# Kernel optimization log

Measured on AMD Instinct MI355X. Metric: run time of the kernel, lower is better.

The kernel has to match this reference:

```python
import jax, jax.numpy as jnp
import numpy as np

N = 512      # nodes
E = 512      # edges = nb-graph nodes
M = 16384    # nb-graph edges
FIN = 64     # in_node_nf
HID = 128    # hidden_nf
D = 32       # VTV_coord_nf (positional-encoding width)


def _silu(v):
    return v * jax.nn.sigmoid(v)


def _mlp(v, w1, b1, w2, b2):
    # 2-layer MLP with SiLU (matches MLP(in, out, [hidden]))
    return _silu(v @ w1 + b1) @ w2 + b2


def setup_inputs() -> dict:
    key = jax.random.key(0)
    ks = jax.random.split(key, 32)

    def lin(k, i, o, scale=None):
        s = (1.0 / np.sqrt(i)) if scale is None else scale
        return jax.random.normal(k, (i, o), dtype=jnp.float32) * jnp.float32(s)

    inp = {}
    inp['h'] = jax.random.normal(ks[0], (N, FIN), dtype=jnp.float32)
    inp['x'] = jax.random.normal(ks[1], (N, 3), dtype=jnp.float32)
    inp['edges'] = jax.random.randint(ks[2], (2, E), 0, N)
    inp['nb_edge'] = jax.random.randint(ks[3], (2, M), 0, E)
    inp['edge_attr'] = jax.random.normal(ks[4], (E, 4), dtype=jnp.float32)
    inp['nb_num_nodes'] = E  # python int (static)
    # edge_encoder: MLP(2*FIN -> HID -> FIN)
    inp['ew1'] = lin(ks[5], 2 * FIN, HID); inp['eb1'] = jnp.zeros((HID,), jnp.float32)
    inp['ew2'] = lin(ks[6], HID, FIN);     inp['eb2'] = jnp.zeros((FIN,), jnp.float32)
    # PPGN mlp1 / mlp2: MLP(D+FIN -> HID -> FIN)
    inp['p1w1'] = lin(ks[7], D + FIN, HID); inp['p1b1'] = jnp.zeros((HID,), jnp.float32)
    inp['p1w2'] = lin(ks[8], HID, FIN);     inp['p1b2'] = jnp.zeros((FIN,), jnp.float32)
    inp['p2w1'] = lin(ks[9], D + FIN, HID); inp['p2b1'] = jnp.zeros((HID,), jnp.float32)
    inp['p2w2'] = lin(ks[10], HID, FIN);    inp['p2b2'] = jnp.zeros((FIN,), jnp.float32)
    # PPGN output mlp: MLP(D+FIN+FIN -> HID -> FIN) on concat(skip, matmul)
    inp['p3w1'] = lin(ks[11], D + 2 * FIN, HID); inp['p3b1'] = jnp.zeros((HID,), jnp.float32)
    inp['p3w2'] = lin(ks[12], HID, FIN);         inp['p3b2'] = jnp.zeros((FIN,), jnp.float32)
    # IGN 2->1: linear over 5 basis ops
    inp['ign_w'] = lin(ks[13], 5 * FIN, FIN); inp['ign_b'] = jnp.zeros((FIN,), jnp.float32)
    # coord_mlp: Linear(FIN,HID), SiLU, Linear(HID,1,bias=False) with tiny init
    inp['cw1'] = lin(ks[14], FIN, HID); inp['cb1'] = jnp.zeros((HID,), jnp.float32)
    inp['cw2'] = lin(ks[15], HID, 1, scale=0.001)
    # node_dec: MLP(FIN -> HID -> FIN)
    inp['ndw1'] = lin(ks[16], FIN, HID); inp['ndb1'] = jnp.zeros((HID,), jnp.float32)
    inp['ndw2'] = lin(ks[17], HID, FIN); inp['ndb2'] = jnp.zeros((FIN,), jnp.float32)
    return inp


def reference(h, x, edges, nb_edge, edge_attr, nb_num_nodes,
              ew1, eb1, ew2, eb2,
              p1w1, p1b1, p1w2, p1b2,
              p2w1, p2b1, p2w2, p2b2,
              p3w1, p3b1, p3w2, p3b2,
              ign_w, ign_b,
              cw1, cb1, cw2,
              ndw1, ndb1, ndw2, ndb2):
    rows, cols = edges[0], edges[1]
    coord_diff = x[rows] - x[cols]                      # [E,3]
    nbr, nbc = nb_edge[0], nb_edge[1]
    # VTV: inner product of the two relative-position vectors of paired edges
    vtv = jnp.sum(coord_diff[nbr] * coord_diff[nbc], axis=-1)   # [M]
    # sinusoidal positional encoding, a_scale = D/2
    half = D // 2
    div_term = jnp.exp(jnp.log(jnp.float32(10000.0)) * (2.0 * jnp.arange(half, dtype=jnp.float32) / D))
    ang = vtv[:, None] * jnp.float32(D / 2) / div_term          # [M, D/2]
    pe = jnp.stack([jnp.sin(ang), jnp.cos(ang)], axis=-1).reshape(vtv.shape[0], D)
    # node-pair features per original edge
    efn = _mlp(jnp.concatenate([h[rows], h[cols]], axis=1), ew1, eb1, ew2, eb2)  # [E,FIN]
    nb_feat = jnp.concatenate([pe, efn[nbr] * efn[nbc]], axis=1)                 # [M, D+FIN]
    # densify nb-graph 2-tensor and run PPGN block
    En = nb_num_nodes
    T = jnp.zeros((En, En, nb_feat.shape[1]), dtype=nb_feat.dtype).at[nbr, nbc].add(nb_feat)
    m1 = _mlp(T, p1w1, p1b1, p1w2, p1b2)                 # [En,En,FIN]
    m2 = _mlp(T, p2w1, p2b1, p2w2, p2b2)
    mult = jnp.einsum('ikf,kjf->ijf', m1, m2)            # feature-wise matmul
    Tout = _mlp(jnp.concatenate([T, mult], axis=-1), p3w1, p3b1, p3w2, p3b2)
    # IGN 2->1: diag, row-sum, col-sum, total-sum, trace (broadcast)
    idx = jnp.arange(En)
    diag = Tout[idx, idx]                                # [En,FIN]
    rowsum = Tout.sum(axis=1)
    colsum = Tout.sum(axis=0)
    tot = jnp.broadcast_to(Tout.sum(axis=(0, 1)), diag.shape)
    tr = jnp.broadcast_to(diag.sum(axis=0), diag.shape)
    nb_t1 = jnp.concatenate([diag, rowsum, colsum, tot, tr], axis=1) @ ign_w + ign_b  # [En,FIN]
    # coord update: weighted coord_diff, segment-mean over source node
    w = _silu(nb_t1 @ cw1 + cb1) @ cw2                   # [E,1]
    trans = coord_diff * w
    Nn = x.shape[0]
    seg = jax.ops.segment_sum(trans, rows, num_segments=Nn)
    cnt = jax.ops.segment_sum(jnp.ones((rows.shape[0], 1), trans.dtype), rows, num_segments=Nn)
    x_new = x + seg / jnp.clip(cnt, 1.0)
    # node update: scatter_add edge features then residual MLP
    nb_t0 = jax.ops.segment_sum(nb_t1, rows, num_segments=Nn)
    h_new = h + _mlp(nb_t0, ndw1, ndb1, ndw2, ndb2)
    return (h_new, x_new, edge_attr)
```

## Files before the change

kernel.cpp:

```cpp
#include <hip/hip_runtime.h>
#include <hip/hip_bf16.h>

#define NN   512
#define EE   512
#define MM   16384

typedef float v4f __attribute__((ext_vector_type(4)));
typedef short short8v __attribute__((ext_vector_type(8)));

__device__ __forceinline__ float silu_f(float v) { return v / (1.0f + __expf(-v)); }

__global__ __launch_bounds__(128) void k_edge(
    const float* __restrict__ h, const float* __restrict__ x,
    const int* __restrict__ edges,
    const float* __restrict__ ew1, const float* __restrict__ eb1,
    const float* __restrict__ ew2, const float* __restrict__ eb2,
    float* __restrict__ coord_diff, float* __restrict__ efn) {
  __shared__ float hin[128];
  __shared__ float hs[128];
  int e = blockIdx.x;
  int t = threadIdx.x;
  int r = edges[e], c = edges[EE + e];
  if (t < 3) coord_diff[e * 3 + t] = x[r * 3 + t] - x[c * 3 + t];
  if (t < 64) { hin[t] = h[r * 64 + t]; hin[64 + t] = h[c * 64 + t]; }
  __syncthreads();
  float acc = eb1[t];
  for (int k = 0; k < 128; ++k) acc += hin[k] * ew1[k * 128 + t];
  hs[t] = silu_f(acc);
  __syncthreads();
  if (t < 64) {
    float o = eb2[t];
    for (int k = 0; k < 128; ++k) o += hs[k] * ew2[k * 64 + t];
    efn[e * 64 + t] = o;
  }
}

__global__ __launch_bounds__(128) void k_consts(
    const float* __restrict__ p1b1, const float* __restrict__ p1w2, const float* __restrict__ p1b2,
    const float* __restrict__ p2b1, const float* __restrict__ p2w2, const float* __restrict__ p2b2,
    float* __restrict__ c1, float* __restrict__ c2) {
  __shared__ float h1[128], h2[128];
  int t = threadIdx.x;
  h1[t] = silu_f(p1b1[t]); h2[t] = silu_f(p2b1[t]);
  __syncthreads();
  if (t < 64) {
    float a1 = p1b2[t], a2 = p2b2[t];
    for (int k = 0; k < 128; ++k) { a1 += h1[k] * p1w2[k * 64 + t]; a2 += h2[k] * p2w2[k * 64 + t]; }
    c1[t] = a1; c2[t] = a2;
  }
}

__global__ __launch_bounds__(256) void k_prep(const float* __restrict__ p3w1,
                                              __hip_bfloat16* __restrict__ Wt) {
  int e = blockIdx.x * 256 + threadIdx.x;
  int hh = e >> 6, f = e & 63;
  Wt[hh * 64 + f] = __float2bfloat16(p3w1[(96 + f) * 128 + hh]);
}

__global__ __launch_bounds__(256) void k_mark(const int* __restrict__ nb_edge,
                                              int* __restrict__ slotmap) {
  int m = blockIdx.x * 256 + threadIdx.x;
  if (m >= MM) return;
  int cell = nb_edge[m] * 512 + nb_edge[MM + m];
  atomicCAS(&slotmap[cell], -1, -2);
}

__global__ __launch_bounds__(256) void k_compact(int* __restrict__ slotmap,
                                                 int* __restrict__ cells,
                                                 int* __restrict__ nC) {
  int cell = blockIdx.x * 256 + threadIdx.x;
  if (slotmap[cell] != -2) return;
  int s = atomicAdd(nC, 1);
  slotmap[cell] = s;
  cells[s] = cell;
}

__global__ __launch_bounds__(192) void k_scatterT(
    const int* __restrict__ nb_edge, const int* __restrict__ slotmap,
    const float* __restrict__ coord_diff, const float* __restrict__ efn,
    float* __restrict__ Tc) {
  int t = threadIdx.x;
  int sub = (t >= 96) ? 1 : 0;
  int c = t - sub * 96;
  int m = blockIdx.x * 2 + sub;
  int a = nb_edge[m], b = nb_edge[MM + m];
  int s = slotmap[a * 512 + b];
  float val;
  if (c < 32) {
    float vtv = coord_diff[a * 3 + 0] * coord_diff[b * 3 + 0]
              + coord_diff[a * 3 + 1] * coord_diff[b * 3 + 1]
              + coord_diff[a * 3 + 2] * coord_diff[b * 3 + 2];
    int i = c >> 1;
    float ang = vtv * 16.0f * __expf(-0.57564627324851143f * (float)i);
    val = (c & 1) ? cosf(ang) : sinf(ang);
  } else {
    int f = c - 32;
    val = efn[a * 64 + f] * efn[b * 64 + f];
  }
  atomicAdd(&Tc[s * 96 + c], val);
}

__global__ __launch_bounds__(128) void k_mlp96b(
    const int* __restrict__ cells, const int* __restrict__ nC, const float* __restrict__ Tc,
    const float* __restrict__ w11, const float* __restrict__ b11,
    const float* __restrict__ w12, const float* __restrict__ b12,
    const float* __restrict__ w21, const float* __restrict__ b21,
    const float* __restrict__ w22, const float* __restrict__ b22,
    const float* __restrict__ c1, const float* __restrict__ c2,
    const float* __restrict__ p3w1,
    __hip_bfloat16* __restrict__ D1d, __hip_bfloat16* __restrict__ D2dT,
    float* __restrict__ A, float* __restrict__ B,
    float* __restrict__ TWc) {
  __shared__ float xsT[96 * 8];
  __shared__ float hid[8][128];
  __shared__ int cl[8];
  int t = threadIdx.x;
  int nc = *nC;
  int s0 = blockIdx.x * 8;
  if (s0 >= nc) return;
  for (int e = t; e < 768; e += 128) xsT[(e % 96) * 8 + e / 96] = Tc[s0 * 96 + e];
  if (t < 8) cl[t] = (s0 + t < nc) ? cells[s0 + t] : 0;
  __syncthreads();
  float tw[8], a1[8], a2[8];
#pragma unroll
  for (int c = 0; c < 8; ++c) { tw[c] = 0.f; a1[c] = b11[t]; a2[c] = b21[t]; }
  for (int k = 0; k < 96; ++k) {
    float wt = p3w1[k * 128 + t];
    float w1v = w11[k * 128 + t];
    float w2v = w21[k * 128 + t];
    float4 xlo = *(const float4*)&xsT[k * 8];
    float4 xhi = *(const float4*)&xsT[k * 8 + 4];
    float xv[8] = {xlo.x, xlo.y, xlo.z, xlo.w, xhi.x, xhi.y, xhi.z, xhi.w};
#pragma unroll
    for (int c = 0; c < 8; ++c) {
      tw[c] += xv[c] * wt; a1[c] += xv[c] * w1v; a2[c] += xv[c] * w2v;
    }
  }
#pragma unroll
  for (int c = 0; c < 8; ++c) {
    if (s0 + c < nc) TWc[(s0 + c) * 128 + t] = tw[c];
    hid[c][t] = silu_f(a1[c]);
  }
  __syncthreads();
  {
    int hh = t & 63, cq = t >> 6;
    float o[4];
#pragma unroll
    for (int cc = 0; cc < 4; ++cc) o[cc] = b12[hh];
    for (int k = 0; k < 128; ++k) {
      float w = w12[k * 64 + hh];
#pragma unroll
      for (int cc = 0; cc < 4; ++cc) o[cc] += hid[cq * 4 + cc][k] * w;
    }
#pragma unroll
    for (int cc = 0; cc < 4; ++cc) {
      int c = cq * 4 + cc;
      if (s0 + c < nc) {
        float d = o[cc] - c1[hh];
        int cell = cl[c];
        int ai = cell >> 9, bj = cell & 511;
        atomicAdd(&A[ai * 64 + hh], d);
        D1d[(hh * 512 + ai) * 512 + bj] = __float2bfloat16(d);
      }
    }
  }
  __syncthreads();
#pragma unroll
  for (int c = 0; c < 8; ++c) hid[c][t] = silu_f(a2[c]);
  __syncthreads();
  {
    int hh = t & 63, cq = t >> 6;
    float o[4];
#pragma unroll
    for (int cc = 0; cc < 4; ++cc) o[cc] = b22[hh];
    for (int k = 0; k < 128; ++k) {
      float w = w22[k * 64 + hh];
#pragma unroll
      for (int cc = 0; cc < 4; ++cc) o[cc] += hid[cq * 4 + cc][k] * w;
    }
#pragma unroll
    for (int cc = 0; cc < 4; ++cc) {
      int c = cq * 4 + cc;
      if (s0 + c < nc) {
        float d = o[cc] - c2[hh];
        int cell = cl[c];
        int ai = cell >> 9, bj = cell & 511;
        atomicAdd(&B[bj * 64 + hh], d);
        D2dT[(hh * 512 + bj) * 512 + ai] = __float2bfloat16(d);
      }
    }
  }
}

__global__ __launch_bounds__(128) void k_uv(
    const float* __restrict__ A, const float* __restrict__ B,
    const float* __restrict__ c1, const float* __restrict__ c2,
    const float* __restrict__ p3w1, const float* __restrict__ p3b1,
    float* __restrict__ u, float* __restrict__ v) {
  __shared__ float vec[64];
  int i = blockIdx.x, y = blockIdx.y, t = threadIdx.x;
  if (t < 64)
    vec[t] = (y == 0) ? (512.0f * c1[t] * c2[t] + c2[t] * A[i * 64 + t])
                      : (c1[t] * B[i * 64 + t]);
  __syncthreads();
  float a = (y == 0) ? p3b1[t] : 0.f;
  for (int f = 0; f < 64; ++f) a += vec[f] * p3w1[(96 + f) * 128 + t];
  (y == 0 ? u : v)[i * 128 + t] = a;
}

__global__ __launch_bounds__(256) void k_einsum_mfma(
    const __hip_bfloat16* __restrict__ D1d,
    const __hip_bfloat16* __restrict__ D2dT,
    __hip_bfloat16* __restrict__ S_fij) {
  __shared__ short As[128 * 40];
  __shared__ short Bs[128 * 40];
  int b = blockIdx.x;
  int f = b >> 4;
  int i0 = ((b >> 2) & 3) * 128, j0 = (b & 3) * 128;
  int t = threadIdx.x;
  int w = t >> 6, lane = t & 63;
  int wy = w >> 1, wx = w & 1;
  int q = lane >> 4, l15 = lane & 15;
  const short* Ap = (const short*)D1d + f * 262144;
  const short* Bp = (const short*)D2dT + f * 262144;
  int row = t >> 1, seg = t & 1;
  v4f acc[4][4];
#pragma unroll
  for (int yi = 0; yi < 4; ++yi)
#pragma unroll
    for (int xj = 0; xj < 4; ++xj) acc[yi][xj] = (v4f){0.f, 0.f, 0.f, 0.f};
  for (int k0 = 0; k0 < 512; k0 += 32) {
    __syncthreads();
    const short8v* ga = (const short8v*)&Ap[(i0 + row) * 512 + k0 + seg * 16];
    const short8v* gb = (const short8v*)&Bp[(j0 + row) * 512 + k0 + seg * 16];
    *(short8v*)&As[row * 40 + seg * 16] = ga[0];
    *(short8v*)&As[row * 40 + seg * 16 + 8] = ga[1];
    *(short8v*)&Bs[row * 40 + seg * 16] = gb[0];
    *(short8v*)&Bs[row * 40 + seg * 16 + 8] = gb[1];
    __syncthreads();
    short8v af[4], bf[4];
#pragma unroll
    for (int x = 0; x < 4; ++x) {
      af[x] = *(const short8v*)&As[(wy * 64 + x * 16 + l15) * 40 + q * 8];
      bf[x] = *(const short8v*)&Bs[(wx * 64 + x * 16 + l15) * 40 + q * 8];
    }
#pragma unroll
    for (int yi = 0; yi < 4; ++yi)
#pragma unroll
      for (int xj = 0; xj < 4; ++xj)
        acc[yi][xj] = __builtin_amdgcn_mfma_f32_16x16x32_bf16(af[yi], bf[xj], acc[yi][xj], 0, 0, 0);
  }
#pragma unroll
  for (int yi = 0; yi < 4; ++yi)
#pragma unroll
    for (int r = 0; r < 4; ++r) {
      int irow = i0 + wy * 64 + yi * 16 + q * 4 + r;
#pragma unroll
      for (int xj = 0; xj < 4; ++xj)
        S_fij[(f * 512 + irow) * 512 + j0 + wx * 64 + xj * 16 + l15] =
            __float2bfloat16(acc[yi][xj][r]);
    }
}

__global__ __launch_bounds__(256) void k_transpose(
    const __hip_bfloat16* __restrict__ S_fij, __hip_bfloat16* __restrict__ S) {
  __shared__ short lds[64 * 72];
  int t = threadIdx.x;
  int ij0 = blockIdx.x * 64;
  const short* src = (const short*)S_fij;
#pragma unroll
  for (int p = 0; p < 2; ++p) {
    int f = p * 32 + (t >> 3), seg = t & 7;
    short8v ga = *(const short8v*)&src[f * 262144 + ij0 + seg * 8];
    int fgrp = f >> 3, flo = f & 7;
#pragma unroll
    for (int k = 0; k < 8; ++k) {
      int ij = seg * 8 + k;
      int swz = (fgrp ^ (ij & 7) ^ ((ij >> 3) & 7)) & 7;
      lds[ij * 72 + swz * 8 + flo] = ga[k];
    }
  }
  __syncthreads();
  short* dst = (short*)S;
#pragma unroll
  for (int p = 0; p < 2; ++p) {
    int ij = p * 32 + (t >> 3), fseg = t & 7;
    int swz = (fseg ^ (ij & 7) ^ ((ij >> 3) & 7)) & 7;
    short8v val = *(const short8v*)&lds[ij * 72 + swz * 8];
    *(short8v*)&dst[(ij0 + ij) * 64 + fseg * 8] = val;
  }
}

__global__ __launch_bounds__(256) void k_tout_mfma(
    const __hip_bfloat16* __restrict__ S, const float* __restrict__ u,
    const float* __restrict__ v, const float* __restrict__ TWc,
    const int* __restrict__ slotmap, const __hip_bfloat16* __restrict__ Wt,
    float* __restrict__ row_part, float* __restrict__ col_part,
    float* __restrict__ diag_silu) {
  __shared__ __hip_bfloat16 WtL[128 * 72];
  __shared__ __hip_bfloat16 uvL[4096];
  __shared__ __hip_bfloat16 colbuf[4][16][140];
  __shared__ int slotL[256];
  int t = threadIdx.x;
  int w = t >> 6, lane = t & 63;
  int q = lane >> 4, l15 = lane & 15;
  int bi = blockIdx.x >> 5, bj = blockIdx.x & 31;
  int i0 = bi * 16, j0 = bj * 16;
  for (int e = t; e < 4096; e += 256) {
    int row = e >> 5, c2 = e & 31;
    ((unsigned*)WtL)[row * 36 + c2] = ((const unsigned*)Wt)[row * 32 + c2];
  }
  for (int e = t; e < 2048; e += 256)
    uvL[e] = __float2bfloat16(u[(i0 + (e >> 7)) * 128 + (e & 127)]);
  for (int e = t; e < 2048; e += 256)
    uvL[2048 + e] = __float2bfloat16(v[(j0 + (e >> 7)) * 128 + (e & 127)]);
  slotL[t] = slotmap[(i0 + (t >> 4)) * 512 + j0 + (t & 15)];
  short8v a[4][2];
#pragma unroll
  for (int mt = 0; mt < 4; ++mt) {
    const short8v* sp =
        (const short8v*)&S[((i0 + w * 4 + mt) * 512 + j0 + l15) * 64];
    a[mt][0] = sp[q];
    a[mt][1] = sp[4 + q];
  }
  __syncthreads();
#pragma unroll
  for (int half = 0; half < 2; ++half) {
    v4f acc[4][4];
#pragma unroll
    for (int mt = 0; mt < 4; ++mt)
#pragma unroll
      for (int n4 = 0; n4 < 4; ++n4) {
        int nt = half * 4 + n4;
        const short8v* b0 = (const short8v*)&WtL[(nt * 16 + l15) * 72 + q * 8];
        const short8v* b1 = (const short8v*)&WtL[(nt * 16 + l15) * 72 + 32 + q * 8];
        v4f c = {0.f, 0.f, 0.f, 0.f};
        c = __builtin_amdgcn_mfma_f32_16x16x32_bf16(a[mt][0], *b0, c, 0, 0, 0);
        c = __builtin_amdgcn_mfma_f32_16x16x32_bf16(a[mt][1], *b1, c, 0, 0, 0);
        acc[mt][n4] = c;
      }
#pragma unroll
    for (int n4 = 0; n4 < 4; ++n4) {
      int nt = half * 4 + n4;
      int hh = nt * 16 + l15;
      float rs[4] = {0.f, 0.f, 0.f, 0.f};
#pragma unroll
      for (int r = 0; r < 4; ++r) {
        int jL = q * 4 + r;
        float cs = 0.f;
        float vv = __bfloat162float(uvL[2048 + jL * 128 + hh]);
#pragma unroll
        for (int mt = 0; mt < 4; ++mt) {
          int iL = w * 4 + mt;
          float z = acc[mt][n4][r] + __bfloat162float(uvL[iL * 128 + hh]) + vv;
          int s = slotL[iL * 16 + jL];
          if (s >= 0) z += TWc[s * 128 + hh];
          float sv = silu_f(z);
          rs[mt] += sv;
          cs += sv;
          if (bi == bj && iL == jL) diag_silu[(i0 + iL) * 128 + hh] = sv;
        }
        colbuf[w][jL][hh] = __float2bfloat16(cs);
      }
#pragma unroll
      for (int mt = 0; mt < 4; ++mt) {
        float rsum = rs[mt];
        rsum += __shfl_xor(rsum, 16);
        rsum += __shfl_xor(rsum, 32);
        if (q == 0)
          row_part[(bj * 512 + i0 + w * 4 + mt) * 128 + hh] = rsum;
      }
    }
  }
  __syncthreads();
  for (int e = t; e < 2048; e += 256) {
    int jL = e >> 7, hh = e & 127;
    float acc4 = __bfloat162float(colbuf[0][jL][hh]) + __bfloat162float(colbuf[1][jL][hh]) +
                 __bfloat162float(colbuf[2][jL][hh]) + __bfloat162float(colbuf[3][jL][hh]);
    col_part[(bi * 512 + j0 + jL) * 128 + hh] = acc4;
  }
}

__global__ __launch_bounds__(256) void k_sumparts(
    const float* __restrict__ row_part, const float* __restrict__ col_part,
    float* __restrict__ rowsum, float* __restrict__ colsum) {
  int i = blockIdx.x, t = threadIdx.x;
  const float* src = (t < 128) ? row_part : col_part;
  float* dst = (t < 128) ? rowsum : colsum;
  int hc = t & 127;
  float a = 0.f;
  for (int p = 0; p < 32; ++p) a += src[(p * 512 + i) * 128 + hc];
  dst[i * 128 + hc] = a;
}

__global__ __launch_bounds__(64) void k_tout2(
    const float* __restrict__ diag_silu, const float* __restrict__ rowsum_silu,
    const float* __restrict__ colsum_silu,
    const float* __restrict__ w2, const float* __restrict__ b2,
    float* __restrict__ diag_T, float* __restrict__ row_T, float* __restrict__ col_T) {
  __shared__ float in[128];
  int e = blockIdx.x, which = blockIdx.y, t = threadIdx.x;
  const float* src = (which == 0) ? diag_silu : (which == 1) ? rowsum_silu : colsum_silu;
  in[t] = src[e * 128 + t]; in[64 + t] = src[e * 128 + 64 + t];
  __syncthreads();
  float a = 0.f;
  for (int k = 0; k < 128; ++k) a += in[k] * w2[k * 64 + t];
  float bias = b2[t] * ((which == 0) ? 1.0f : 512.0f);
  float* dst = (which == 0) ? diag_T : (which == 1) ? row_T : col_T;
  dst[e * 64 + t] = a + bias;
}

__global__ __launch_bounds__(128) void k_totr(
    const float* __restrict__ row_T, const float* __restrict__ diag_T,
    float* __restrict__ tot, float* __restrict__ tr) {
  int t = threadIdx.x;
  const float* src = (t < 64) ? row_T : diag_T;
  int f = t & 63;
  float a = 0.f;
  for (int e = 0; e < 512; ++e) a += src[e * 64 + f];
  if (t < 64) tot[f] = a; else tr[f] = a;
}

__global__ __launch_bounds__(64) void k_nbt1(
    const float* __restrict__ diag_T, const float* __restrict__ row_T,
    const float* __restrict__ col_T, const float* __restrict__ tot,
    const float* __restrict__ tr,
    const float* __restrict__ gw, const float* __restrict__ gb,
    float* __restrict__ nb_t1) {
  __shared__ float in[320];
  int e = blockIdx.x, t = threadIdx.x;
  in[t] = diag_T[e * 64 + t]; in[64 + t] = row_T[e * 64 + t];
  in[128 + t] = col_T[e * 64 + t]; in[192 + t] = tot[t]; in[256 + t] = tr[t];
  __syncthreads();
  float a = gb[t];
  for (int k = 0; k < 320; ++k) a += in[k] * gw[k * 64 + t];
  nb_t1[e * 64 + t] = a;
}

__global__ __launch_bounds__(128) void k_edge_out(
    const int* __restrict__ edges, const float* __restrict__ coord_diff,
    const float* __restrict__ nb_t1, const float* __restrict__ edge_attr,
    const float* __restrict__ cw1, const float* __restrict__ cb1,
    const float* __restrict__ cw2,
    float* __restrict__ seg, float* __restrict__ cnt, float* __restrict__ nb_t0,
    float* __restrict__ out_ea) {
  __shared__ float in[64];
  __shared__ float red[128];
  int e = blockIdx.x, t = threadIdx.x;
  if (t < 64) in[t] = nb_t1[e * 64 + t];
  __syncthreads();
  float a = cb1[t];
  for (int k = 0; k < 64; ++k) a += in[k] * cw1[k * 128 + t];
  red[t] = silu_f(a) * cw2[t];
  __syncthreads();
  for (int s2 = 64; s2 > 0; s2 >>= 1) {
    if (t < s2) red[t] += red[t + s2];
    __syncthreads();
  }
  float w = red[0];
  int r = edges[e];
  if (t < 3) atomicAdd(&seg[r * 3 + t], coord_diff[e * 3 + t] * w);
  if (t == 64) atomicAdd(&cnt[r], 1.0f);
  if (t < 64) atomicAdd(&nb_t0[r * 64 + t], in[t]);
  if (t < 4) out_ea[e * 4 + t] = edge_attr[e * 4 + t];
}

__global__ __launch_bounds__(128) void k_node_out(
    const float* __restrict__ h, const float* __restrict__ x,
    const float* __restrict__ seg, const float* __restrict__ cnt,
    const float* __restrict__ nb_t0,
    const float* __restrict__ w1, const float* __restrict__ b1,
    const float* __restrict__ w2, const float* __restrict__ b2,
    float* __restrict__ out_h, float* __restrict__ out_x) {
  __shared__ float in[64];
  __shared__ float hs[128];
  int n = blockIdx.x, t = threadIdx.x;
  if (t < 3) {
    float c = cnt[n]; if (c < 1.f) c = 1.f;
    out_x[n * 3 + t] = x[n * 3 + t] + seg[n * 3 + t] / c;
  }
  if (t < 64) in[t] = nb_t0[n * 64 + t];
  __syncthreads();
  float a = b1[t];
  for (int k = 0; k < 64; ++k) a += in[k] * w1[k * 128 + t];
  hs[t] = silu_f(a);
  __syncthreads();
  if (t < 64) {
    float o = b2[t];
    for (int k = 0; k < 128; ++k) o += hs[k] * w2[k * 64 + t];
    out_h[n * 64 + t] = h[n * 64 + t] + o;
  }
}

extern "C" void kernel_launch(void* const* d_in, const int* in_sizes, int n_in,
                              void* d_out, int out_size, void* d_ws, size_t ws_size,
                              hipStream_t stream) {
  (void)in_sizes; (void)n_in; (void)out_size; (void)ws_size;
  const float* h  = (const float*)d_in[0];
  const float* x  = (const float*)d_in[1];
  const int* edges   = (const int*)d_in[2];
  const int* nb_edge = (const int*)d_in[3];
  const float* edge_attr = (const float*)d_in[4];
  const float* ew1 = (const float*)d_in[6],  *eb1 = (const float*)d_in[7];
  const float* ew2 = (const float*)d_in[8],  *eb2 = (const float*)d_in[9];
  const float* p1w1 = (const float*)d_in[10], *p1b1 = (const float*)d_in[11];
  const float* p1w2 = (const float*)d_in[12], *p1b2 = (const float*)d_in[13];
  const float* p2w1 = (const float*)d_in[14], *p2b1 = (const float*)d_in[15];
  const float* p2w2 = (const float*)d_in[16], *p2b2 = (const float*)d_in[17];
  const float* p3w1 = (const float*)d_in[18], *p3b1 = (const float*)d_in[19];
  const float* p3w2 = (const float*)d_in[20], *p3b2 = (const float*)d_in[21];
  const float* ignw = (const float*)d_in[22], *ignb = (const float*)d_in[23];
  const float* cw1 = (const float*)d_in[24], *cb1 = (const float*)d_in[25];
  const float* cw2 = (const float*)d_in[26];
  const float* ndw1 = (const float*)d_in[27], *ndb1 = (const float*)d_in[28];
  const float* ndw2 = (const float*)d_in[29], *ndb2 = (const float*)d_in[30];

  char* ws = (char*)d_ws;
  __hip_bfloat16* D1d  = (__hip_bfloat16*)(ws + 0);
  __hip_bfloat16* S    = (__hip_bfloat16*)(ws + 0);
  __hip_bfloat16* D2dT = (__hip_bfloat16*)(ws + 33554432);
  __hip_bfloat16* S_fij = (__hip_bfloat16*)(ws + 67108864);
  float* row_part = (float*)(ws + 100663296);
  float* col_part = (float*)(ws + 117440512);
  float* Tc    = (float*)(ws + 134217728);
  int*   nC    = (int*)(ws + 140509184);
  float* A     = (float*)(ws + 140509200);
  float* B     = (float*)(ws + 140640272);
  float* seg   = (float*)(ws + 140771344);
  float* cnt   = (float*)(ws + 140777488);
  float* nb_t0 = (float*)(ws + 140779536);
  int*   slotmap  = (int*)(ws + 140910608);
  int*   cells    = (int*)(ws + 143007760);
  float* TWc      = (float*)(ws + 151461904);
  float* c1       = (float*)(ws + 159850512);
  float* c2       = (float*)(ws + 159850768);
  float* u        = (float*)(ws + 159851024);
  float* v        = (float*)(ws + 160113168);
  float* coord_diff  = (float*)(ws + 160375312);
  float* efn         = (float*)(ws + 160381456);
  float* diag_silu   = (float*)(ws + 160512528);
  float* rowsum_silu = (float*)(ws + 160774672);
  float* colsum_silu = (float*)(ws + 161036816);
  float* diag_T      = (float*)(ws + 161298960);
  float* row_T       = (float*)(ws + 161430032);
  float* col_T       = (float*)(ws + 161561104);
  float* tot         = (float*)(ws + 161692176);
  float* tr          = (float*)(ws + 161692432);
  float* nb_t1       = (float*)(ws + 161692688);
  __hip_bfloat16* Wt  = (__hip_bfloat16*)(ws + 161823760);

  float* out_h  = (float*)d_out;
  float* out_x  = out_h + 512 * 64;
  float* out_ea = out_x + 512 * 3;

  hipMemsetAsync(ws, 0, 67108864, stream);
  hipMemsetAsync(slotmap, 0xFF, 1048576, stream);
  hipMemsetAsync(ws + 134217728, 0, 6692880, stream);

  k_edge<<<512, 128, 0, stream>>>(h, x, edges, ew1, eb1, ew2, eb2, coord_diff, efn);
  k_consts<<<1, 128, 0, stream>>>(p1b1, p1w2, p1b2, p2b1, p2w2, p2b2, c1, c2);
  k_prep<<<32, 256, 0, stream>>>(p3w1, Wt);
  k_mark<<<64, 256, 0, stream>>>(nb_edge, slotmap);
  k_compact<<<1024, 256, 0, stream>>>(slotmap, cells, nC);
  k_scatterT<<<8192, 192, 0, stream>>>(nb_edge, slotmap, coord_diff, efn, Tc);
  k_mlp96b<<<2048, 128, 0, stream>>>(cells, nC, Tc,
                                     p1w1, p1b1, p1w2, p1b2,
                                     p2w1, p2b1, p2w2, p2b2,
                                     c1, c2, p3w1, D1d, D2dT, A, B, TWc);
  k_uv<<<dim3(512, 2), 128, 0, stream>>>(A, B, c1, c2, p3w1, p3b1, u, v);
  k_einsum_mfma<<<1024, 256, 0, stream>>>(D1d, D2dT, S_fij);
  k_transpose<<<4096, 256, 0, stream>>>(S_fij, S);
  k_tout_mfma<<<1024, 256, 0, stream>>>(S, u, v, TWc, slotmap, Wt,
                                        row_part, col_part, diag_silu);
  k_sumparts<<<512, 256, 0, stream>>>(row_part, col_part, rowsum_silu, colsum_silu);
  k_tout2<<<dim3(512, 3), 64, 0, stream>>>(diag_silu, rowsum_silu, colsum_silu,
                                           p3w2, p3b2, diag_T, row_T, col_T);
  k_totr<<<1, 128, 0, stream>>>(row_T, diag_T, tot, tr);
  k_nbt1<<<512, 64, 0, stream>>>(diag_T, row_T, col_T, tot, tr, ignw, ignb, nb_t1);
  k_edge_out<<<512, 128, 0, stream>>>(edges, coord_diff, nb_t1, edge_attr,
                                      cw1, cb1, cw2, seg, cnt, nb_t0, out_ea);
  k_node_out<<<512, 128, 0, stream>>>(h, x, seg, cnt, nb_t0,
                                      ndw1, ndb1, ndw2, ndb2, out_h, out_x);
}
```

Before: 414.3 us.

## Move per-cell PPGN MLPs to bf16 MFMA with concatenated weight matrices

Replaces the scalar FP32 per-cell MLP kernel (8 cells per block) with a bf16 MFMA kernel that handles 64 cells per block. It concatenates p3w1/p1w1/p2w1 into one transposed bf16 matrix and both second-layer weights into another, and converts Tc to bf16 in a separate kernel. The goal is to cut the FP32 FMA cost of the three first-layer projections and two second-layer projections. In exchange it adds bf16 rounding on the inputs, hidden activations and TWc, plus two extra launches.

```diff
diff --git a/kernel.cpp b/kernel.cpp
--- a/kernel.cpp
+++ b/kernel.cpp
@@ -55,6 +55,25 @@
   int e = blockIdx.x * 256 + threadIdx.x;
   int hh = e >> 6, f = e & 63;
   Wt[hh * 64 + f] = __float2bfloat16(p3w1[(96 + f) * 128 + hh]);
+}
+
+__global__ __launch_bounds__(256) void k_prepw2(
+    const float* __restrict__ w11, const float* __restrict__ w21,
+    const float* __restrict__ p3w1,
+    const float* __restrict__ w12, const float* __restrict__ w22,
+    __hip_bfloat16* __restrict__ W1cat, __hip_bfloat16* __restrict__ W2cat) {
+  int e = blockIdx.x * 256 + threadIdx.x;
+  if (e < 36864) {
+    int n = e / 96, k = e % 96;
+    const float* src = (n < 128) ? p3w1 : (n < 256) ? w11 : w21;
+    int nn = (n < 128) ? n : (n < 256) ? n - 128 : n - 256;
+    W1cat[e] = __float2bfloat16(src[k * 128 + nn]);
+  } else if (e < 53248) {
+    int e2 = e - 36864;
+    int n = e2 >> 7, k = e2 & 127;
+    const float* src = (n < 64) ? w12 : w22;
+    W2cat[e2] = __float2bfloat16(src[k * 64 + (n & 63)]);
+  }
 }
 
 __global__ __launch_bounds__(256) void k_mark(const int* __restrict__ nb_edge,
@@ -100,93 +119,110 @@
   atomicAdd(&Tc[s * 96 + c], val);
 }
 
-__global__ __launch_bounds__(128) void k_mlp96b(
-    const int* __restrict__ cells, const int* __restrict__ nC, const float* __restrict__ Tc,
-    const float* __restrict__ w11, const float* __restrict__ b11,
-    const float* __restrict__ w12, const float* __restrict__ b12,
-    const float* __restrict__ w21, const float* __restrict__ b21,
-    const float* __restrict__ w22, const float* __restrict__ b22,
+__global__ __launch_bounds__(256) void k_cvtT(const float* __restrict__ Tc,
+                                              __hip_bfloat16* __restrict__ Tcb) {
+  int e = blockIdx.x * 256 + threadIdx.x;
+  Tcb[e] = __float2bfloat16(Tc[e]);
+}
+
+__global__ __launch_bounds__(256) void k_mlp_mfma(
+    const int* __restrict__ cells, const int* __restrict__ nC,
+    const __hip_bfloat16* __restrict__ Tcb,
+    const __hip_bfloat16* __restrict__ W1cat, const __hip_bfloat16* __restrict__ W2cat,
+    const float* __restrict__ b11, const float* __restrict__ b21,
+    const float* __restrict__ b12, const float* __restrict__ b22,
     const float* __restrict__ c1, const float* __restrict__ c2,
-    const float* __restrict__ p3w1,
     __hip_bfloat16* __restrict__ D1d, __hip_bfloat16* __restrict__ D2dT,
     float* __restrict__ A, float* __restrict__ B,
     float* __restrict__ TWc) {
-  __shared__ float xsT[96 * 8];
-  __shared__ float hid[8][128];
-  __shared__ int cl[8];
-  int t = threadIdx.x;
+  __shared__ __hip_bfloat16 hid1[64 * 136];
+  __shared__ __hip_bfloat16 hid2[64 * 136];
+  __shared__ int cl[64];
+  int t = threadIdx.x;
+  int w = t >> 6, lane = t & 63;
+  int q = lane >> 4, l15 = lane & 15;
   int nc = *nC;
-  int s0 = blockIdx.x * 8;
+  int s0 = blockIdx.x * 64;
   if (s0 >= nc) return;
-  for (int e = t; e < 768; e += 128) xsT[(e % 96) * 8 + e / 96] = Tc[s0 * 96 + e];
-  if (t < 8) cl[t] = (s0 + t < nc) ? cells[s0 + t] : 0;
-  __syncthreads();
-  float tw[8], a1[8], a2[8];
-#pragma unroll
-  for (int c = 0; c < 8; ++c) { tw[c] = 0.f; a1[c] = b11[t]; a2[c] = b21[t]; }
-  for (int k = 0; k < 96; ++k) {
-    float wt = p3w1[k * 128 + t];
-    float w1v = w11[k * 128 + t];
-    float w2v = w21[k * 128 + t];
-    float4 xlo = *(const float4*)&xsT[k * 8];
-    float4 xhi = *(const float4*)&xsT[k * 8 + 4];
-    float xv[8] = {xlo.x, xlo.y, xlo.z, xlo.w, xhi.x, xhi.y, xhi.z, xhi.w};
-#pragma unroll
-    for (int c = 0; c < 8; ++c) {
-      tw[c] += xv[c] * wt; a1[c] += xv[c] * w1v; a2[c] += xv[c] * w2v;
-    }
-  }
-#pragma unroll
-  for (int c = 0; c < 8; ++c) {
-    if (s0 + c < nc) TWc[(s0 + c) * 128 + t] = tw[c];
-    hid[c][t] = silu_f(a1[c]);
-  }
-  __syncthreads();
-  {
-    int hh = t & 63, cq = t >> 6;
-    float o[4];
-#pragma unroll
-    for (int cc = 0; cc < 4; ++cc) o[cc] = b12[hh];
-    for (int k = 0; k < 128; ++k) {
-      float w = w12[k * 64 + hh];
-#pragma unroll
-      for (int cc = 0; cc < 4; ++cc) o[cc] += hid[cq * 4 + cc][k] * w;
-    }
-#pragma unroll
-    for (int cc = 0; cc < 4; ++cc) {
-      int c = cq * 4 + cc;
-      if (s0 + c < nc) {
-        float d = o[cc] - c1[hh];
-        int cell = cl[c];
+  if (t < 64) cl[t] = (s0 + t < nc) ? cells[s0 + t] : 0;
+  int cellA = s0 + w * 16 + l15;
+  const short* tp = (const short*)Tcb + cellA * 96;
+  short8v af[3];
+#pragma unroll
+  for (int ks = 0; ks < 3; ++ks) af[ks] = *(const short8v*)&tp[ks * 32 + q * 8];
+  __syncthreads();
+  v4f acc[24];
+#pragma unroll
+  for (int nt = 0; nt < 24; ++nt) acc[nt] = (v4f){0.f, 0.f, 0.f, 0.f};
+  const short* w1p = (const short*)W1cat;
+#pragma unroll
+  for (int ks = 0; ks < 3; ++ks)
+#pragma unroll
+    for (int nt = 0; nt < 24; ++nt) {
+      short8v bf = *(const short8v*)&w1p[(nt * 16 + l15) * 96 + ks * 32 + q * 8];
+      acc[nt] = __builtin_amdgcn_mfma_f32_16x16x32_bf16(af[ks], bf, acc[nt], 0, 0, 0);
+    }
+#pragma unroll
+  for (int nt = 0; nt < 8; ++nt) {
+    int hh = nt * 16 + l15;
+#pragma unroll
+    for (int r = 0; r < 4; ++r) {
+      int s = s0 + w * 16 + q * 4 + r;
+      if (s < nc) TWc[s * 128 + hh] = acc[nt][r];
+    }
+  }
+#pragma unroll
+  for (int nt = 8; nt < 16; ++nt) {
+    int hh = (nt - 8) * 16 + l15;
+    float bb = b11[hh];
+#pragma unroll
+    for (int r = 0; r < 4; ++r)
+      hid1[(w * 16 + q * 4 + r) * 136 + hh] = __float2bfloat16(silu_f(acc[nt][r] + bb));
+  }
+#pragma unroll
+  for (int nt = 16; nt < 24; ++nt) {
+    int hh = (nt - 16) * 16 + l15;
+    float bb = b21[hh];
+#pragma unroll
+    for (int r = 0; r < 4; ++r)
+      hid2[(w * 16 + q * 4 + r) * 136 + hh] = __float2bfloat16(silu_f(acc[nt][r] + bb));
+  }
+  const short* w2p = (const short*)W2cat;
+  const short* h1p = (const short*)hid1;
+  const short* h2p = (const short*)hid2;
+  v4f acc2[8];
+#pragma unroll
+  for (int nt = 0; nt < 8; ++nt) acc2[nt] = (v4f){0.f, 0.f, 0.f, 0.f};
+#pragma unroll
+  for (int ks = 0; ks < 4; ++ks) {
+    short8v af1 = *(const short8v*)&h1p[(w * 16 + l15) * 136 + ks * 32 + q * 8];
+    short8v af2 = *(const short8v*)&h2p[(w * 16 + l15) * 136 + ks * 32 + q * 8];
+#pragma unroll
+    for (int nt = 0; nt < 4; ++nt) {
+      short8v bf1 = *(const short8v*)&w2p[(nt * 16 + l15) * 128 + ks * 32 + q * 8];
+      short8v bf2 = *(const short8v*)&w2p[(64 + nt * 16 + l15) * 128 + ks * 32 + q * 8];
+      acc2[nt] = __builtin_amdgcn_mfma_f32_16x16x32_bf16(af1, bf1, acc2[nt], 0, 0, 0);
+      acc2[4 + nt] = __builtin_amdgcn_mfma_f32_16x16x32_bf16(af2, bf2, acc2[4 + nt], 0, 0, 0);
+    }
+  }
+#pragma unroll
+  for (int nt = 0; nt < 4; ++nt) {
+    int hh = nt * 16 + l15;
+    float bb1 = b12[hh] - c1[hh];
+    float bb2 = b22[hh] - c2[hh];
+#pragma unroll
+    for (int r = 0; r < 4; ++r) {
+      int m = w * 16 + q * 4 + r;
+      int s = s0 + m;
+      if (s < nc) {
+        int cell = cl[m];
         int ai = cell >> 9, bj = cell & 511;
-        atomicAdd(&A[ai * 64 + hh], d);
-        D1d[(hh * 512 + ai) * 512 + bj] = __float2bfloat16(d);
-      }
-    }
-  }
-  __syncthreads();
-#pragma unroll
-  for (int c = 0; c < 8; ++c) hid[c][t] = silu_f(a2[c]);
-  __syncthreads();
-  {
-    int hh = t & 63, cq = t >> 6;
-    float o[4];
-#pragma unroll
-    for (int cc = 0; cc < 4; ++cc) o[cc] = b22[hh];
-    for (int k = 0; k < 128; ++k) {
-      float w = w22[k * 64 + hh];
-#pragma unroll
-      for (int cc = 0; cc < 4; ++cc) o[cc] += hid[cq * 4 + cc][k] * w;
-    }
-#pragma unroll
-    for (int cc = 0; cc < 4; ++cc) {
-      int c = cq * 4 + cc;
-      if (s0 + c < nc) {
-        float d = o[cc] - c2[hh];
-        int cell = cl[c];
-        int ai = cell >> 9, bj = cell & 511;
-        atomicAdd(&B[bj * 64 + hh], d);
-        D2dT[(hh * 512 + bj) * 512 + ai] = __float2bfloat16(d);
+        float d1 = acc2[nt][r] + bb1;
+        atomicAdd(&A[ai * 64 + hh], d1);
+        D1d[(hh * 512 + ai) * 512 + bj] = __float2bfloat16(d1);
+        float d2 = acc2[4 + nt][r] + bb2;
+        atomicAdd(&B[bj * 64 + hh], d2);
+        D2dT[(hh * 512 + bj) * 512 + ai] = __float2bfloat16(d2);
       }
     }
   }
@@ -547,7 +583,10 @@
   float* tot         = (float*)(ws + 161692176);
   float* tr          = (float*)(ws + 161692432);
   float* nb_t1       = (float*)(ws + 161692688);
-  __hip_bfloat16* Wt  = (__hip_bfloat16*)(ws + 161823760);
+  __hip_bfloat16* Wt    = (__hip_bfloat16*)(ws + 161823760);
+  __hip_bfloat16* Tcb   = (__hip_bfloat16*)(ws + 161840144);
+  __hip_bfloat16* W1cat = (__hip_bfloat16*)(ws + 164985872);
+  __hip_bfloat16* W2cat = (__hip_bfloat16*)(ws + 165059600);
 
   float* out_h  = (float*)d_out;
   float* out_x  = out_h + 512 * 64;
@@ -560,13 +599,14 @@
   k_edge<<<512, 128, 0, stream>>>(h, x, edges, ew1, eb1, ew2, eb2, coord_diff, efn);
   k_consts<<<1, 128, 0, stream>>>(p1b1, p1w2, p1b2, p2b1, p2w2, p2b2, c1, c2);
   k_prep<<<32, 256, 0, stream>>>(p3w1, Wt);
+  k_prepw2<<<208, 256, 0, stream>>>(p1w1, p2w1, p3w1, p1w2, p2w2, W1cat, W2cat);
   k_mark<<<64, 256, 0, stream>>>(nb_edge, slotmap);
   k_compact<<<1024, 256, 0, stream>>>(slotmap, cells, nC);
   k_scatterT<<<8192, 192, 0, stream>>>(nb_edge, slotmap, coord_diff, efn, Tc);
-  k_mlp96b<<<2048, 128, 0, stream>>>(cells, nC, Tc,
-                                     p1w1, p1b1, p1w2, p1b2,
-                                     p2w1, p2b1, p2w2, p2b2,
-                                     c1, c2, p3w1, D1d, D2dT, A, B, TWc);
+  k_cvtT<<<6144, 256, 0, stream>>>(Tc, Tcb);
+  k_mlp_mfma<<<256, 256, 0, stream>>>(cells, nC, Tcb, W1cat, W2cat,
+                                      p1b1, p2b1, p1b2, p2b2, c1, c2,
+                                      D1d, D2dT, A, B, TWc);
   k_uv<<<dim3(512, 2), 128, 0, stream>>>(A, B, c1, c2, p3w1, p3b1, u, v);
   k_einsum_mfma<<<1024, 256, 0, stream>>>(D1d, D2dT, S_fij);
   k_transpose<<<4096, 256, 0, stream>>>(S_fij, S);
```

Result: no change. 414.5 us (+0.1%).
